# Kernel optimization log

Measured on AMD Instinct MI355X. Metric: run time of the kernel, lower is better.

## Reference

```python
import jax, jax.numpy as jnp
import numpy as np

B, D, N, H = 1024, 512, 16, 512  # batch, latent, branches, hidden


def _lrelu(v):
    return jnp.where(v >= 0, v, 0.1 * v)  # LeakyReLU(0.1)


def setup_inputs() -> dict:
    key = jax.random.key(0)
    ks = jax.random.split(key, 9)
    s = 0.02
    return {
        "x": jax.random.normal(ks[0], (B, D, N), dtype=jnp.float32),
        "Ws1": jax.random.normal(ks[1], (D, D), dtype=jnp.float32) * s,
        "bs1": jnp.zeros((D,), dtype=jnp.float32),
        "Ws2": jax.random.normal(ks[2], (D, D), dtype=jnp.float32) * s,
        "bs2": jnp.zeros((D,), dtype=jnp.float32),
        # per-branch binary classifiers: Linear(D,H)+LeakyReLU+Linear(H,1)
        "Wc1": jax.random.normal(ks[3], (N, D, H), dtype=jnp.float32) * s,
        "bc1": jnp.zeros((N, H), dtype=jnp.float32),
        "Wc2": jax.random.normal(ks[4], (N, H), dtype=jnp.float32) * s,
        "bc2": jnp.zeros((N,), dtype=jnp.float32),
    }


def reference(x, Ws1, bs1, Ws2, bs2, Wc1, bc1, Wc2, bc2):
    # x: [B, D, N] -> per-branch tokens [B, N, D]
    xb = jnp.transpose(x, (0, 2, 1))
    # shared MLP applied to every branch slice (same weights)
    h = _lrelu(xb @ Ws1 + bs1)
    shared = _lrelu(h @ Ws2 + bs2)  # [B, N, D]
    # per-branch classifier on its own branch slice -> sigmoid probs
    h1 = _lrelu(jnp.einsum('bnd,ndh->bnh', shared, Wc1) + bc1)
    logits = jnp.einsum('bnh,nh->bn', h1, Wc2) + bc2  # [B, N]
    out = jax.nn.sigmoid(logits)[:, None, :]  # [B, 1, N]
    # full pass: concat branch slices along batch (branch-major), every
    # classifier applied to the full stack -> raw logits
    full_in = jnp.transpose(shared, (1, 0, 2)).reshape(N * B, D)  # [M, D]
    h2 = _lrelu(jnp.einsum('md,ndh->mnh', full_in, Wc1) + bc1)  # [M, N, H]
    full_logits = jnp.einsum('mnh,nh->mn', h2, Wc2) + bc2  # [M, N]
    full_out = full_logits[:, None, :]  # [N*B, 1, N]
    return (out, full_out)
```

## Files before the change

### kernel.cpp

```cpp
#include <hip/hip_runtime.h>
#include <hip/hip_bf16.h>
#include <stdint.h>

#define Bq 1024
#define Dq 512
#define Nq 16
#define Hq 512
#define Mq (Bq*Nq)

typedef short v8s  __attribute__((ext_vector_type(8)));
typedef float v4f  __attribute__((ext_vector_type(4)));
typedef float v16f __attribute__((ext_vector_type(16)));

typedef __attribute__((address_space(3))) unsigned int as3_u32;
typedef __attribute__((address_space(1))) const unsigned int as1_u32;

#define VMCNT(n) asm volatile("s_waitcnt vmcnt(" #n ")" ::: "memory")

__device__ __forceinline__ unsigned short f2bf(float f) {
  union { float f; unsigned u; } v; v.f = f;
  return (unsigned short)((v.u + 0x7fffu + ((v.u >> 16) & 1u)) >> 16);
}

__global__ void k_transpose_x(const float* __restrict__ x, unsigned short* __restrict__ xb) {
  __shared__ float lds[Dq][Nq + 1];
  const int b = blockIdx.x;
  const float* xi = x + (size_t)b * Dq * Nq;
  const int t = threadIdx.x;
  for (int p = 0; p < (Dq*Nq)/256; ++p) {
    int i = t + p*256;
    lds[i >> 4][i & (Nq-1)] = xi[i];
  }
  __syncthreads();
  unsigned short* o = xb + (size_t)b * Nq * Dq;
  for (int p = 0; p < (Dq*Nq)/256; ++p) {
    int i = t + p*256;
    o[i] = f2bf(lds[i & (Dq-1)][i >> 9]);
  }
}

__global__ void k_transpose_w(const float* __restrict__ Ws1, const float* __restrict__ Ws2,
                              const float* __restrict__ Wc1,
                              unsigned short* __restrict__ Ws1t, unsigned short* __restrict__ Ws2t,
                              unsigned short* __restrict__ Wc1t) {
  __shared__ float tile[32][33];
  const int z = blockIdx.z;
  const float* in;
  unsigned short* out;
  if (z == 0)      { in = Ws1; out = Ws1t; }
  else if (z == 1) { in = Ws2; out = Ws2t; }
  else             { in = Wc1 + (size_t)(z-2) * 512 * 512; out = Wc1t + (size_t)(z-2) * 512 * 512; }
  const int tx = threadIdx.x, ty = threadIdx.y;
  const int c0 = blockIdx.x * 32, r0 = blockIdx.y * 32;
#pragma unroll
  for (int j = 0; j < 4; ++j)
    tile[ty + j*8][tx] = in[(size_t)(r0 + ty + j*8) * 512 + c0 + tx];
  __syncthreads();
#pragma unroll
  for (int j = 0; j < 4; ++j) {
    int c = c0 + ty + j*8;
    int r = r0 + tx;
    out[(size_t)c * 512 + r] = f2bf(tile[tx][ty + j*8]);
  }
}

template<int MODE, int BM>
__global__ __launch_bounds__(256, 2)
void k_gemm(const unsigned short* __restrict__ A,
            const unsigned short* __restrict__ Bt,
            const float* __restrict__ bias,
            void* __restrict__ out_,
            const float* __restrict__ w2,
            int permute) {
  constexpr int BN = 128, BK = 32, KD = 512;
  constexpr int NI = (BM == 256) ? 4 : 2;
  constexpr int AG = BM / 16;
  constexpr int TG = AG + BN / 16;
  __shared__ __align__(16) unsigned short As[2][BM][BK];
  __shared__ __align__(16) unsigned short Bs[2][BN][BK];

  const int t = threadIdx.x;
  const int wave = t >> 6, lane = t & 63;
  const int wr = (BM == 256) ? wave : (wave >> 1);
  const int wc = (BM == 256) ? 0    : (wave & 1);
  const int l32 = lane & 31, kh0 = lane >> 5;
  const int bm = blockIdx.x * BM, bn = blockIdx.y * BN;
  const int z = blockIdx.z;

  const unsigned short* Bz = Bt + (size_t)z * KD * 512;
  const float* biasz = bias + (size_t)z * 512;

  const int lrow = lane >> 2;
  const int lslot = lane & 3;

  auto stage = [&](int buf, int kt) {
#pragma unroll
    for (int i = wave; i < TG; i += 4) {
      const int isA = (i < AG);
      const int r0 = (isA ? i : i - AG) * 16;
      const int row = r0 + lrow;
      const int cg = lslot ^ ((row >> 1) & 3);
      const unsigned short* g = isA ? &A [(size_t)(bm + row) * KD + kt*BK + cg*8]
                                    : &Bz[(size_t)(bn + row) * KD + kt*BK + cg*8];
      as3_u32* d = isA ? (as3_u32*)&As[buf][r0][0] : (as3_u32*)&Bs[buf][r0][0];
      __builtin_amdgcn_global_load_lds((as1_u32*)g, d, 16, 0, 0);
    }
  };

  v16f acc[2][NI] = {};

  stage(0, 0);
  __syncthreads();

  for (int kt = 0; kt < KD / BK; ++kt) {
    const int cur = kt & 1;
    if (kt + 1 < KD / BK) stage(cur ^ 1, kt + 1);

    v8s af[2][2], bf[NI][2];
#pragma unroll
    for (int mi = 0; mi < 2; ++mi) {
      int ra = wr*64 + mi*32 + l32;
#pragma unroll
      for (int kh = 0; kh < 2; ++kh) {
        int c = kh*2 + kh0;
        af[mi][kh] = *(const v8s*)&As[cur][ra][(c ^ ((ra >> 1) & 3)) * 8];
      }
    }
#pragma unroll
    for (int ni = 0; ni < NI; ++ni) {
      int rb = wc*64 + ni*32 + l32;
#pragma unroll
      for (int kh = 0; kh < 2; ++kh) {
        int c = kh*2 + kh0;
        bf[ni][kh] = *(const v8s*)&Bs[cur][rb][(c ^ ((rb >> 1) & 3)) * 8];
      }
    }
#pragma unroll
    for (int kh = 0; kh < 2; ++kh)
#pragma unroll
      for (int mi = 0; mi < 2; ++mi)
#pragma unroll
        for (int ni = 0; ni < NI; ++ni)
          acc[mi][ni] = __builtin_amdgcn_mfma_f32_32x32x16_bf16(af[mi][kh], bf[ni][kh], acc[mi][ni], 0, 0, 0);
    __syncthreads();
  }

  if (MODE == 0) {
    unsigned short* O = (unsigned short*)out_;
#pragma unroll
    for (int mi = 0; mi < 2; ++mi) {
#pragma unroll
      for (int ni = 0; ni < NI; ++ni) {
        int col = bn + wc*64 + ni*32 + l32;
        float bcol = biasz[col];
#pragma unroll
        for (int reg = 0; reg < 16; ++reg) {
          int rl = (reg & 3) + 8*(reg >> 2) + 4*kh0;
          int grow = bm + wr*64 + mi*32 + rl;
          int orow = permute ? ((grow & 15) * Bq + (grow >> 4)) : grow;
          float v = acc[mi][ni][reg] + bcol;
          v = v >= 0.f ? v : 0.1f * v;
          O[(size_t)orow * 512 + col] = f2bf(v);
        }
      }
    }
  } else {
    float* FL = (float*)out_;
    const float* w2z = w2 + (size_t)z * 512;
#pragma unroll
    for (int mi = 0; mi < 2; ++mi) {
#pragma unroll
      for (int reg = 0; reg < 16; ++reg) {
        int rl = (reg & 3) + 8*(reg >> 2) + 4*kh0;
        float s = 0.f;
#pragma unroll
        for (int ni = 0; ni < NI; ++ni) {
          int col = bn + ni*32 + l32;
          float v = acc[mi][ni][reg] + biasz[col];
          v = v >= 0.f ? v : 0.1f * v;
          s += v * w2z[col];
        }
#pragma unroll
        for (int off = 1; off < 32; off <<= 1)
          s += __shfl_xor(s, off, 64);
        if (l32 == 0) {
          int grow = bm + wave*64 + mi*32 + rl;
          atomicAdd(&FL[(size_t)grow * Nq + z], s);
        }
      }
    }
  }
}

__global__ __launch_bounds__(256, 3)
void k_headgemm(const unsigned short* __restrict__ A,
                const unsigned short* __restrict__ Bt,
                const float* __restrict__ bias,
                float* __restrict__ FL,
                const float* __restrict__ w2) {
  __shared__ __align__(16) unsigned short As[3][128][32];
  __shared__ __align__(16) unsigned short Bs[3][128][32];

  const int t = threadIdx.x;
  const int wave = t >> 6, lane = t & 63;
  const int wr = wave >> 1, wc = wave & 1;
  const int fr = lane & 15, fq = lane >> 4;

  const int bid = blockIdx.x;
  const int lin = (bid & 7) * 1024 + (bid >> 3);
  const int bm = (lin & 127) * 128;
  const int bn = ((lin >> 7) & 3) * 128;
  const int z  = lin >> 9;

  const unsigned short* Bz = Bt + (size_t)z * Dq * 512;
  const float* biasz = bias + (size_t)z * 512;
  const float* w2z   = w2   + (size_t)z * 512;

  const int sr = lane >> 2;
  const int sc = (lane & 3) ^ ((sr >> 1) & 3);
  const unsigned short* aSrc = A  + (size_t)(bm + wave*32 + sr) * Dq + sc*8;
  const unsigned short* bSrc = Bz + (size_t)(bn + wave*32 + sr) * Dq + sc*8;
  char* dstA = (char*)As + (wave*32) * 64;
  char* dstB = (char*)Bs + (wave*32) * 64;

  auto stage = [&](int T, int slot) {
    if (T >= 16) return;
#pragma unroll
    for (int j = 0; j < 2; ++j) {
      __builtin_amdgcn_global_load_lds((as1_u32*)(aSrc + T*32 + (size_t)j*16*Dq),
                                       (as3_u32*)(dstA + slot*8192 + j*1024), 16, 0, 0);
      __builtin_amdgcn_global_load_lds((as1_u32*)(bSrc + T*32 + (size_t)j*16*Dq),
                                       (as3_u32*)(dstB + slot*8192 + j*1024), 16, 0, 0);
    }
  };

  const int swz = (fq ^ ((fr >> 1) & 3)) * 16;
  int offA[4], offB[4];
#pragma unroll
  for (int mi = 0; mi < 4; ++mi) offA[mi] = (wr*64 + mi*16 + fr) * 64 + swz;
#pragma unroll
  for (int ni = 0; ni < 4; ++ni) offB[ni] = (wc*64 + ni*16 + fr) * 64 + swz;

  v4f acc[4][4] = {};

  stage(0, 0);
  stage(1, 1);
  VMCNT(4);
  __builtin_amdgcn_s_barrier();
  __builtin_amdgcn_sched_barrier(0);

  int sR = 0, sS = 2;
  for (int kt = 0; kt < 16; ++kt) {
    stage(kt + 2, sS);

    const char* aB = (const char*)As + sR * 8192;
    const char* bB = (const char*)Bs + sR * 8192;
    v8s af[4], bf[4];
#pragma unroll
    for (int i = 0; i < 4; ++i) af[i] = *(const v8s*)(aB + offA[i]);
#pragma unroll
    for (int i = 0; i < 4; ++i) bf[i] = *(const v8s*)(bB + offB[i]);

    __builtin_amdgcn_s_setprio(1);
#pragma unroll
    for (int mi = 0; mi < 4; ++mi)
#pragma unroll
      for (int ni = 0; ni < 4; ++ni)
        acc[mi][ni] = __builtin_amdgcn_mfma_f32_16x16x32_bf16(af[mi], bf[ni], acc[mi][ni], 0, 0, 0);
    __builtin_amdgcn_s_setprio(0);

    if (kt < 14)       { VMCNT(4); }
    else if (kt == 14) { VMCNT(0); }
    if (kt < 15) {
      __builtin_amdgcn_s_barrier();
      __builtin_amdgcn_sched_barrier(0);
    }
    sR = (sR + 1 == 3) ? 0 : sR + 1;
    sS = (sS + 1 == 3) ? 0 : sS + 1;
  }

  float bcol[4], wcol[4];
#pragma unroll
  for (int ni = 0; ni < 4; ++ni) {
    int col = bn + wc*64 + ni*16 + fr;
    bcol[ni] = biasz[col];
    wcol[ni] = w2z[col];
  }
#pragma unroll
  for (int mi = 0; mi < 4; ++mi) {
#pragma unroll
    for (int reg = 0; reg < 4; ++reg) {
      float s = 0.f;
#pragma unroll
      for (int ni = 0; ni < 4; ++ni) {
        float v = acc[mi][ni][reg] + bcol[ni];
        v = v >= 0.f ? v : 0.1f * v;
        s += v * wcol[ni];
      }
#pragma unroll
      for (int off = 1; off < 16; off <<= 1)
        s += __shfl_xor(s, off, 64);
      if (fr == 0) {
        int grow = bm + wr*64 + mi*16 + fq*4 + reg;
        atomicAdd(&FL[(size_t)grow * Nq + z], s);
      }
    }
  }
}

__global__ void k_final(const float* __restrict__ fl, const float* __restrict__ bc2,
                        float* __restrict__ out) {
  int i = blockIdx.x * 256 + threadIdx.x;
  int m = i >> 4, n = i & 15;
  float v = fl[i] + bc2[n];
  out[Mq + i] = v;
  if (n == (m >> 10)) {
    int b = m & (Bq - 1);
    out[b * Nq + n] = 1.f / (1.f + __expf(-v));
  }
}

extern "C" void kernel_launch(void* const* d_in, const int* in_sizes, int n_in,
                              void* d_out, int out_size, void* d_ws, size_t ws_size,
                              hipStream_t stream) {
  (void)in_sizes; (void)n_in; (void)out_size; (void)ws_size;
  const float* x   = (const float*)d_in[0];
  const float* Ws1 = (const float*)d_in[1];
  const float* bs1 = (const float*)d_in[2];
  const float* Ws2 = (const float*)d_in[3];
  const float* bs2 = (const float*)d_in[4];
  const float* Wc1 = (const float*)d_in[5];
  const float* bc1 = (const float*)d_in[6];
  const float* Wc2 = (const float*)d_in[7];
  const float* bc2 = (const float*)d_in[8];

  char* ws = (char*)d_ws;
  unsigned short* Xb   = (unsigned short*)(ws);
  unsigned short* Hbuf = (unsigned short*)(ws + (size_t)16*1024*1024);
  unsigned short* Sm   = (unsigned short*)(ws + (size_t)32*1024*1024);
  unsigned short* Ws1t = (unsigned short*)(ws + (size_t)48*1024*1024);
  unsigned short* Ws2t = (unsigned short*)(ws + (size_t)48*1024*1024 + 512*1024);
  unsigned short* Wc1t = (unsigned short*)(ws + (size_t)49*1024*1024);
  float*          FL   = (float*)         (ws + (size_t)57*1024*1024);

  hipMemsetAsync(FL, 0, (size_t)Mq * Nq * sizeof(float), stream);

  k_transpose_x<<<Bq, 256, 0, stream>>>(x, Xb);
  k_transpose_w<<<dim3(16,16,18), dim3(32,8), 0, stream>>>(Ws1, Ws2, Wc1, Ws1t, Ws2t, Wc1t);

  k_gemm<0,128><<<dim3(128,4,1), 256, 0, stream>>>(Xb,   Ws1t, bs1, Hbuf, nullptr, 0);
  k_gemm<0,128><<<dim3(128,4,1), 256, 0, stream>>>(Hbuf, Ws2t, bs2, Sm,   nullptr, 1);
  k_headgemm<<<8192, 256, 0, stream>>>(Sm, Wc1t, bc1, FL, Wc2);

  k_final<<<(Mq*Nq)/256, 256, 0, stream>>>(FL, bc2, (float*)d_out);
}
```

Measured before the change: 351.2 us.

## Enlarge head GEMM tile to 256x128 and switch to 32x32x16 MFMA

The head GEMM block tile grows from 128x128 to 256x128, so each wave computes a 128x64 sub-tile using 32x32x16 bf16 MFMAs in place of 16x16x32. This gives more reuse of each loaded B fragment and fewer LDS reads per MFMA. The LDS double/triple buffers grow to match, and occupancy drops from 3 to 2 blocks per CU. The launch moves from an XCD-swizzled linear grid to a plain 3D grid, which may change L2 locality of the shared B tiles.

```diff
diff --git a/kernel.cpp b/kernel.cpp
--- a/kernel.cpp
+++ b/kernel.cpp
@@ -192,25 +192,23 @@
   }
 }
 
-__global__ __launch_bounds__(256, 3)
+__global__ __launch_bounds__(256, 2)
 void k_headgemm(const unsigned short* __restrict__ A,
                 const unsigned short* __restrict__ Bt,
                 const float* __restrict__ bias,
                 float* __restrict__ FL,
                 const float* __restrict__ w2) {
-  __shared__ __align__(16) unsigned short As[3][128][32];
+  __shared__ __align__(16) unsigned short As[3][256][32];
   __shared__ __align__(16) unsigned short Bs[3][128][32];
 
   const int t = threadIdx.x;
   const int wave = t >> 6, lane = t & 63;
   const int wr = wave >> 1, wc = wave & 1;
-  const int fr = lane & 15, fq = lane >> 4;
-
-  const int bid = blockIdx.x;
-  const int lin = (bid & 7) * 1024 + (bid >> 3);
-  const int bm = (lin & 127) * 128;
-  const int bn = ((lin >> 7) & 3) * 128;
-  const int z  = lin >> 9;
+  const int l32 = lane & 31, kh0 = lane >> 5;
+
+  const int bm = blockIdx.x * 256;
+  const int bn = blockIdx.y * 128;
+  const int z  = blockIdx.z;
 
   const unsigned short* Bz = Bt + (size_t)z * Dq * 512;
   const float* biasz = bias + (size_t)z * 512;
@@ -218,34 +216,44 @@
 
   const int sr = lane >> 2;
   const int sc = (lane & 3) ^ ((sr >> 1) & 3);
-  const unsigned short* aSrc = A  + (size_t)(bm + wave*32 + sr) * Dq + sc*8;
+  const unsigned short* aSrc = A  + (size_t)(bm + wave*64 + sr) * Dq + sc*8;
   const unsigned short* bSrc = Bz + (size_t)(bn + wave*32 + sr) * Dq + sc*8;
-  char* dstA = (char*)As + (wave*32) * 64;
+  char* dstA = (char*)As + (wave*64) * 64;
   char* dstB = (char*)Bs + (wave*32) * 64;
 
   auto stage = [&](int T, int slot) {
     if (T >= 16) return;
 #pragma unroll
-    for (int j = 0; j < 2; ++j) {
+    for (int j = 0; j < 4; ++j)
       __builtin_amdgcn_global_load_lds((as1_u32*)(aSrc + T*32 + (size_t)j*16*Dq),
-                                       (as3_u32*)(dstA + slot*8192 + j*1024), 16, 0, 0);
+                                       (as3_u32*)(dstA + slot*16384 + j*1024), 16, 0, 0);
+#pragma unroll
+    for (int j = 0; j < 2; ++j)
       __builtin_amdgcn_global_load_lds((as1_u32*)(bSrc + T*32 + (size_t)j*16*Dq),
                                        (as3_u32*)(dstB + slot*8192 + j*1024), 16, 0, 0);
-    }
   };
 
-  const int swz = (fq ^ ((fr >> 1) & 3)) * 16;
-  int offA[4], offB[4];
-#pragma unroll
-  for (int mi = 0; mi < 4; ++mi) offA[mi] = (wr*64 + mi*16 + fr) * 64 + swz;
-#pragma unroll
-  for (int ni = 0; ni < 4; ++ni) offB[ni] = (wc*64 + ni*16 + fr) * 64 + swz;
-
-  v4f acc[4][4] = {};
+  int offA[4][2], offB[2][2];
+#pragma unroll
+  for (int mi = 0; mi < 4; ++mi) {
+    int ra = wr*128 + mi*32 + l32;
+#pragma unroll
+    for (int kh = 0; kh < 2; ++kh)
+      offA[mi][kh] = ra*64 + (((kh*2 + kh0) ^ ((ra >> 1) & 3)) * 16);
+  }
+#pragma unroll
+  for (int ni = 0; ni < 2; ++ni) {
+    int rb = wc*64 + ni*32 + l32;
+#pragma unroll
+    for (int kh = 0; kh < 2; ++kh)
+      offB[ni][kh] = rb*64 + (((kh*2 + kh0) ^ ((rb >> 1) & 3)) * 16);
+  }
+
+  v16f acc[4][2] = {};
 
   stage(0, 0);
   stage(1, 1);
-  VMCNT(4);
+  VMCNT(6);
   __builtin_amdgcn_s_barrier();
   __builtin_amdgcn_sched_barrier(0);
 
@@ -253,23 +261,31 @@
   for (int kt = 0; kt < 16; ++kt) {
     stage(kt + 2, sS);
 
-    const char* aB = (const char*)As + sR * 8192;
+    const char* aB = (const char*)As + sR * 16384;
     const char* bB = (const char*)Bs + sR * 8192;
-    v8s af[4], bf[4];
-#pragma unroll
-    for (int i = 0; i < 4; ++i) af[i] = *(const v8s*)(aB + offA[i]);
-#pragma unroll
-    for (int i = 0; i < 4; ++i) bf[i] = *(const v8s*)(bB + offB[i]);
+    v8s af[4][2], bf[2][2];
+#pragma unroll
+    for (int mi = 0; mi < 4; ++mi)
+#pragma unroll
+      for (int kh = 0; kh < 2; ++kh)
+        af[mi][kh] = *(const v8s*)(aB + offA[mi][kh]);
+#pragma unroll
+    for (int ni = 0; ni < 2; ++ni)
+#pragma unroll
+      for (int kh = 0; kh < 2; ++kh)
+        bf[ni][kh] = *(const v8s*)(bB + offB[ni][kh]);
 
     __builtin_amdgcn_s_setprio(1);
 #pragma unroll
-    for (int mi = 0; mi < 4; ++mi)
-#pragma unroll
-      for (int ni = 0; ni < 4; ++ni)
-        acc[mi][ni] = __builtin_amdgcn_mfma_f32_16x16x32_bf16(af[mi], bf[ni], acc[mi][ni], 0, 0, 0);
+    for (int kh = 0; kh < 2; ++kh)
+#pragma unroll
+      for (int mi = 0; mi < 4; ++mi)
+#pragma unroll
+        for (int ni = 0; ni < 2; ++ni)
+          acc[mi][ni] = __builtin_amdgcn_mfma_f32_32x32x16_bf16(af[mi][kh], bf[ni][kh], acc[mi][ni], 0, 0, 0);
     __builtin_amdgcn_s_setprio(0);
 
-    if (kt < 14)       { VMCNT(4); }
+    if (kt < 14)       { VMCNT(6); }
     else if (kt == 14) { VMCNT(0); }
     if (kt < 15) {
       __builtin_amdgcn_s_barrier();
@@ -279,29 +295,30 @@
     sS = (sS + 1 == 3) ? 0 : sS + 1;
   }
 
-  float bcol[4], wcol[4];
-#pragma unroll
-  for (int ni = 0; ni < 4; ++ni) {
-    int col = bn + wc*64 + ni*16 + fr;
+  float bcol[2], wcol[2];
+#pragma unroll
+  for (int ni = 0; ni < 2; ++ni) {
+    int col = bn + wc*64 + ni*32 + l32;
     bcol[ni] = biasz[col];
     wcol[ni] = w2z[col];
   }
 #pragma unroll
   for (int mi = 0; mi < 4; ++mi) {
 #pragma unroll
-    for (int reg = 0; reg < 4; ++reg) {
+    for (int reg = 0; reg < 16; ++reg) {
+      int rl = (reg & 3) + 8*(reg >> 2) + 4*kh0;
       float s = 0.f;
 #pragma unroll
-      for (int ni = 0; ni < 4; ++ni) {
+      for (int ni = 0; ni < 2; ++ni) {
         float v = acc[mi][ni][reg] + bcol[ni];
         v = v >= 0.f ? v : 0.1f * v;
         s += v * wcol[ni];
       }
 #pragma unroll
-      for (int off = 1; off < 16; off <<= 1)
+      for (int off = 1; off < 32; off <<= 1)
         s += __shfl_xor(s, off, 64);
-      if (fr == 0) {
-        int grow = bm + wr*64 + mi*16 + fq*4 + reg;
+      if (l32 == 0) {
+        int grow = bm + wr*128 + mi*32 + rl;
         atomicAdd(&FL[(size_t)grow * Nq + z], s);
       }
     }
@@ -350,7 +367,7 @@
 
   k_gemm<0,128><<<dim3(128,4,1), 256, 0, stream>>>(Xb,   Ws1t, bs1, Hbuf, nullptr, 0);
   k_gemm<0,128><<<dim3(128,4,1), 256, 0, stream>>>(Hbuf, Ws2t, bs2, Sm,   nullptr, 1);
-  k_headgemm<<<8192, 256, 0, stream>>>(Sm, Wc1t, bc1, FL, Wc2);
+  k_headgemm<<<dim3(64,4,16), 256, 0, stream>>>(Sm, Wc1t, bc1, FL, Wc2);
 
   k_final<<<(Mq*Nq)/256, 256, 0, stream>>>(FL, bc2, (float*)d_out);
 }
```

New measurement: 448.3 us. +27.6%, slower.

## Replace triple-buffered headgemm pipeline with single-buffer BK=64 synchronous loop

Applied to the files above, without the earlier changes.

The head GEMM drops its three-slot async global-to-LDS pipeline with explicit vmcnt waits. It now uses a single 128x64 LDS tile per operand, loaded and consumed each K step between two __syncthreads, with a new XOR swizzle over 8 chunks. The block-id remap that grouped tiles by weight slice is removed in favour of a plain 3D grid, and the occupancy hint in launch_bounds is dropped. This simplifies the code and halves the number of K iterations, but it gives up overlapping loads with MFMA work and may lose L2 locality from the old tile ordering.

```diff
diff --git a/kernel.cpp b/kernel.cpp
--- a/kernel.cpp
+++ b/kernel.cpp
@@ -14,8 +14,6 @@
 
 typedef __attribute__((address_space(3))) unsigned int as3_u32;
 typedef __attribute__((address_space(1))) const unsigned int as1_u32;
-
-#define VMCNT(n) asm volatile("s_waitcnt vmcnt(" #n ")" ::: "memory")
 
 __device__ __forceinline__ unsigned short f2bf(float f) {
   union { float f; unsigned u; } v; v.f = f;
@@ -192,91 +190,80 @@
   }
 }
 
-__global__ __launch_bounds__(256, 3)
+__global__ __launch_bounds__(256)
 void k_headgemm(const unsigned short* __restrict__ A,
                 const unsigned short* __restrict__ Bt,
                 const float* __restrict__ bias,
                 float* __restrict__ FL,
                 const float* __restrict__ w2) {
-  __shared__ __align__(16) unsigned short As[3][128][32];
-  __shared__ __align__(16) unsigned short Bs[3][128][32];
+  __shared__ __align__(16) unsigned short As[128][64];
+  __shared__ __align__(16) unsigned short Bs[128][64];
 
   const int t = threadIdx.x;
   const int wave = t >> 6, lane = t & 63;
   const int wr = wave >> 1, wc = wave & 1;
   const int fr = lane & 15, fq = lane >> 4;
 
-  const int bid = blockIdx.x;
-  const int lin = (bid & 7) * 1024 + (bid >> 3);
-  const int bm = (lin & 127) * 128;
-  const int bn = ((lin >> 7) & 3) * 128;
-  const int z  = lin >> 9;
+  const int bm = blockIdx.x * 128;
+  const int bn = blockIdx.y * 128;
+  const int z  = blockIdx.z;
 
   const unsigned short* Bz = Bt + (size_t)z * Dq * 512;
   const float* biasz = bias + (size_t)z * 512;
   const float* w2z   = w2   + (size_t)z * 512;
 
-  const int sr = lane >> 2;
-  const int sc = (lane & 3) ^ ((sr >> 1) & 3);
-  const unsigned short* aSrc = A  + (size_t)(bm + wave*32 + sr) * Dq + sc*8;
-  const unsigned short* bSrc = Bz + (size_t)(bn + wave*32 + sr) * Dq + sc*8;
-  char* dstA = (char*)As + (wave*32) * 64;
-  char* dstB = (char*)Bs + (wave*32) * 64;
-
-  auto stage = [&](int T, int slot) {
-    if (T >= 16) return;
-#pragma unroll
-    for (int j = 0; j < 2; ++j) {
-      __builtin_amdgcn_global_load_lds((as1_u32*)(aSrc + T*32 + (size_t)j*16*Dq),
-                                       (as3_u32*)(dstA + slot*8192 + j*1024), 16, 0, 0);
-      __builtin_amdgcn_global_load_lds((as1_u32*)(bSrc + T*32 + (size_t)j*16*Dq),
-                                       (as3_u32*)(dstB + slot*8192 + j*1024), 16, 0, 0);
-    }
+  const int sr8 = lane >> 3;
+  const int sc8 = (lane & 7) ^ sr8;
+  const unsigned short* aSrc = A  + (size_t)(bm + wave*32 + sr8) * Dq + sc8*8;
+  const unsigned short* bSrc = Bz + (size_t)(bn + wave*32 + sr8) * Dq + sc8*8;
+
+  auto stage = [&](int kt) {
+#pragma unroll
+    for (int g = 0; g < 4; ++g)
+      __builtin_amdgcn_global_load_lds((as1_u32*)(aSrc + kt*64 + (size_t)g*8*Dq),
+                                       (as3_u32*)&As[wave*32 + g*8][0], 16, 0, 0);
+#pragma unroll
+    for (int g = 0; g < 4; ++g)
+      __builtin_amdgcn_global_load_lds((as1_u32*)(bSrc + kt*64 + (size_t)g*8*Dq),
+                                       (as3_u32*)&Bs[wave*32 + g*8][0], 16, 0, 0);
   };
 
-  const int swz = (fq ^ ((fr >> 1) & 3)) * 16;
-  int offA[4], offB[4];
-#pragma unroll
-  for (int mi = 0; mi < 4; ++mi) offA[mi] = (wr*64 + mi*16 + fr) * 64 + swz;
-#pragma unroll
-  for (int ni = 0; ni < 4; ++ni) offB[ni] = (wc*64 + ni*16 + fr) * 64 + swz;
+  int offA[4][2], offB[4][2];
+#pragma unroll
+  for (int mi = 0; mi < 4; ++mi) {
+    int r = wr*64 + mi*16 + fr;
+#pragma unroll
+    for (int kh = 0; kh < 2; ++kh)
+      offA[mi][kh] = r*128 + (((kh*4 + fq) ^ (fr & 7)) * 16);
+  }
+#pragma unroll
+  for (int ni = 0; ni < 4; ++ni) {
+    int r = wc*64 + ni*16 + fr;
+#pragma unroll
+    for (int kh = 0; kh < 2; ++kh)
+      offB[ni][kh] = r*128 + (((kh*4 + fq) ^ (fr & 7)) * 16);
+  }
 
   v4f acc[4][4] = {};
 
-  stage(0, 0);
-  stage(1, 1);
-  VMCNT(4);
-  __builtin_amdgcn_s_barrier();
-  __builtin_amdgcn_sched_barrier(0);
-
-  int sR = 0, sS = 2;
-  for (int kt = 0; kt < 16; ++kt) {
-    stage(kt + 2, sS);
-
-    const char* aB = (const char*)As + sR * 8192;
-    const char* bB = (const char*)Bs + sR * 8192;
-    v8s af[4], bf[4];
-#pragma unroll
-    for (int i = 0; i < 4; ++i) af[i] = *(const v8s*)(aB + offA[i]);
-#pragma unroll
-    for (int i = 0; i < 4; ++i) bf[i] = *(const v8s*)(bB + offB[i]);
-
-    __builtin_amdgcn_s_setprio(1);
-#pragma unroll
-    for (int mi = 0; mi < 4; ++mi)
-#pragma unroll
-      for (int ni = 0; ni < 4; ++ni)
-        acc[mi][ni] = __builtin_amdgcn_mfma_f32_16x16x32_bf16(af[mi], bf[ni], acc[mi][ni], 0, 0, 0);
-    __builtin_amdgcn_s_setprio(0);
-
-    if (kt < 14)       { VMCNT(4); }
-    else if (kt == 14) { VMCNT(0); }
-    if (kt < 15) {
-      __builtin_amdgcn_s_barrier();
-      __builtin_amdgcn_sched_barrier(0);
-    }
-    sR = (sR + 1 == 3) ? 0 : sR + 1;
-    sS = (sS + 1 == 3) ? 0 : sS + 1;
+  for (int kt = 0; kt < 8; ++kt) {
+    stage(kt);
+    __syncthreads();
+
+#pragma unroll
+    for (int kh = 0; kh < 2; ++kh) {
+      v8s af[4], bf[4];
+#pragma unroll
+      for (int mi = 0; mi < 4; ++mi) af[mi] = *(const v8s*)((const char*)As + offA[mi][kh]);
+#pragma unroll
+      for (int ni = 0; ni < 4; ++ni) bf[ni] = *(const v8s*)((const char*)Bs + offB[ni][kh]);
+#pragma unroll
+      for (int mi = 0; mi < 4; ++mi)
+#pragma unroll
+        for (int ni = 0; ni < 4; ++ni)
+          acc[mi][ni] = __builtin_amdgcn_mfma_f32_16x16x32_bf16(af[mi], bf[ni], acc[mi][ni], 0, 0, 0);
+    }
+    __syncthreads();
   }
 
   float bcol[4], wcol[4];
@@ -350,7 +337,7 @@
 
   k_gemm<0,128><<<dim3(128,4,1), 256, 0, stream>>>(Xb,   Ws1t, bs1, Hbuf, nullptr, 0);
   k_gemm<0,128><<<dim3(128,4,1), 256, 0, stream>>>(Hbuf, Ws2t, bs2, Sm,   nullptr, 1);
-  k_headgemm<<<8192, 256, 0, stream>>>(Sm, Wc1t, bc1, FL, Wc2);
+  k_headgemm<<<dim3(128,4,16), 256, 0, stream>>>(Sm, Wc1t, bc1, FL, Wc2);
 
   k_final<<<(Mq*Nq)/256, 256, 0, stream>>>(FL, bc2, (float*)d_out);
 }
```

New measurement: 321.2 us. -8.5%, faster.

## Enlarge head GEMM tile to 256x256 with 8 waves and 4-stage pipeline

Applied to the files above, without the earlier changes.

Reworks the per-branch head GEMM from 128x128 tiles with 4 waves and a 3-slot LDS ring to 256x256 tiles with 8 waves, each wave computing 128x64, and a 4-slot prefetch ring three tiles deep. The launch becomes a plain 3D grid, dropping the swizzled block-to-tile mapping. The intent is more arithmetic per byte loaded and fewer atomic adds per output row, since each block now covers twice the columns. In exchange it doubles LDS use, allows one block per CU with more registers per thread, adds an extra barrier per K step, and loses the L2-friendly block ordering.

```diff
diff --git a/kernel.cpp b/kernel.cpp
--- a/kernel.cpp
+++ b/kernel.cpp
@@ -192,91 +192,84 @@
   }
 }
 
-__global__ __launch_bounds__(256, 3)
+__global__ __launch_bounds__(512, 1)
 void k_headgemm(const unsigned short* __restrict__ A,
                 const unsigned short* __restrict__ Bt,
                 const float* __restrict__ bias,
                 float* __restrict__ FL,
                 const float* __restrict__ w2) {
-  __shared__ __align__(16) unsigned short As[3][128][32];
-  __shared__ __align__(16) unsigned short Bs[3][128][32];
+  __shared__ __align__(16) unsigned short As[4][256][32];
+  __shared__ __align__(16) unsigned short Bs[4][256][32];
 
   const int t = threadIdx.x;
   const int wave = t >> 6, lane = t & 63;
-  const int wr = wave >> 1, wc = wave & 1;
+  const int wr = wave >> 2, wc = wave & 3;
   const int fr = lane & 15, fq = lane >> 4;
 
-  const int bid = blockIdx.x;
-  const int lin = (bid & 7) * 1024 + (bid >> 3);
-  const int bm = (lin & 127) * 128;
-  const int bn = ((lin >> 7) & 3) * 128;
-  const int z  = lin >> 9;
+  const int bm = blockIdx.x * 256;
+  const int bn = blockIdx.y * 256;
+  const int z  = blockIdx.z;
 
   const unsigned short* Bz = Bt + (size_t)z * Dq * 512;
   const float* biasz = bias + (size_t)z * 512;
   const float* w2z   = w2   + (size_t)z * 512;
 
-  const int sr = lane >> 2;
-  const int sc = (lane & 3) ^ ((sr >> 1) & 3);
-  const unsigned short* aSrc = A  + (size_t)(bm + wave*32 + sr) * Dq + sc*8;
-  const unsigned short* bSrc = Bz + (size_t)(bn + wave*32 + sr) * Dq + sc*8;
-  char* dstA = (char*)As + (wave*32) * 64;
-  char* dstB = (char*)Bs + (wave*32) * 64;
-
-  auto stage = [&](int T, int slot) {
-    if (T >= 16) return;
+  const int srow = t >> 2;
+  const int schunk = (t & 3) ^ ((t >> 3) & 3);
+  const unsigned short* aS = A  + (size_t)(bm + srow) * Dq + schunk*8;
+  const unsigned short* bS = Bz + (size_t)(bn + srow) * Dq + schunk*8;
+
+  auto stageT = [&](int T) {
+    const int s = T & 3;
 #pragma unroll
     for (int j = 0; j < 2; ++j) {
-      __builtin_amdgcn_global_load_lds((as1_u32*)(aSrc + T*32 + (size_t)j*16*Dq),
-                                       (as3_u32*)(dstA + slot*8192 + j*1024), 16, 0, 0);
-      __builtin_amdgcn_global_load_lds((as1_u32*)(bSrc + T*32 + (size_t)j*16*Dq),
-                                       (as3_u32*)(dstB + slot*8192 + j*1024), 16, 0, 0);
+      __builtin_amdgcn_global_load_lds((as1_u32*)(aS + (size_t)j*128*Dq + T*32),
+                                       (as3_u32*)&As[s][j*128 + wave*16][0], 16, 0, 0);
+      __builtin_amdgcn_global_load_lds((as1_u32*)(bS + (size_t)j*128*Dq + T*32),
+                                       (as3_u32*)&Bs[s][j*128 + wave*16][0], 16, 0, 0);
     }
   };
 
   const int swz = (fq ^ ((fr >> 1) & 3)) * 16;
-  int offA[4], offB[4];
-#pragma unroll
-  for (int mi = 0; mi < 4; ++mi) offA[mi] = (wr*64 + mi*16 + fr) * 64 + swz;
-#pragma unroll
-  for (int ni = 0; ni < 4; ++ni) offB[ni] = (wc*64 + ni*16 + fr) * 64 + swz;
-
-  v4f acc[4][4] = {};
-
-  stage(0, 0);
-  stage(1, 1);
+  int offA[8], offB[4];
+#pragma unroll
+  for (int mi = 0; mi < 8; ++mi) offA[mi] = (wr*128 + mi*16 + fr) * 64 + swz;
+#pragma unroll
+  for (int ni = 0; ni < 4; ++ni) offB[ni] = (wc*64  + ni*16 + fr) * 64 + swz;
+
+  v4f acc[8][4] = {};
+
+  stageT(0); stageT(1); stageT(2);
   VMCNT(4);
   __builtin_amdgcn_s_barrier();
   __builtin_amdgcn_sched_barrier(0);
 
-  int sR = 0, sS = 2;
-  for (int kt = 0; kt < 16; ++kt) {
-    stage(kt + 2, sS);
-
-    const char* aB = (const char*)As + sR * 8192;
-    const char* bB = (const char*)Bs + sR * 8192;
-    v8s af[4], bf[4];
-#pragma unroll
-    for (int i = 0; i < 4; ++i) af[i] = *(const v8s*)(aB + offA[i]);
-#pragma unroll
-    for (int i = 0; i < 4; ++i) bf[i] = *(const v8s*)(bB + offB[i]);
+#pragma unroll 4
+  for (int T = 0; T < 16; ++T) {
+    const char* aB = (const char*)&As[T & 3][0][0];
+    const char* bB = (const char*)&Bs[T & 3][0][0];
+    v8s af[8], bf[4];
+#pragma unroll
+    for (int mi = 0; mi < 8; ++mi) af[mi] = *(const v8s*)(aB + offA[mi]);
+#pragma unroll
+    for (int ni = 0; ni < 4; ++ni) bf[ni] = *(const v8s*)(bB + offB[ni]);
+
+    if (T + 3 < 16) stageT(T + 3);
+
+    __builtin_amdgcn_s_barrier();
 
     __builtin_amdgcn_s_setprio(1);
 #pragma unroll
-    for (int mi = 0; mi < 4; ++mi)
+    for (int mi = 0; mi < 8; ++mi)
 #pragma unroll
       for (int ni = 0; ni < 4; ++ni)
         acc[mi][ni] = __builtin_amdgcn_mfma_f32_16x16x32_bf16(af[mi], bf[ni], acc[mi][ni], 0, 0, 0);
     __builtin_amdgcn_s_setprio(0);
 
-    if (kt < 14)       { VMCNT(4); }
-    else if (kt == 14) { VMCNT(0); }
-    if (kt < 15) {
-      __builtin_amdgcn_s_barrier();
-      __builtin_amdgcn_sched_barrier(0);
-    }
-    sR = (sR + 1 == 3) ? 0 : sR + 1;
-    sS = (sS + 1 == 3) ? 0 : sS + 1;
+    if (T < 14)       { VMCNT(4); }
+    else if (T == 14) { VMCNT(0); }
+    __builtin_amdgcn_s_barrier();
+    __builtin_amdgcn_sched_barrier(0);
   }
 
   float bcol[4], wcol[4];
@@ -287,7 +280,7 @@
     wcol[ni] = w2z[col];
   }
 #pragma unroll
-  for (int mi = 0; mi < 4; ++mi) {
+  for (int mi = 0; mi < 8; ++mi) {
 #pragma unroll
     for (int reg = 0; reg < 4; ++reg) {
       float s = 0.f;
@@ -301,7 +294,7 @@
       for (int off = 1; off < 16; off <<= 1)
         s += __shfl_xor(s, off, 64);
       if (fr == 0) {
-        int grow = bm + wr*64 + mi*16 + fq*4 + reg;
+        int grow = bm + wr*128 + mi*16 + fq*4 + reg;
         atomicAdd(&FL[(size_t)grow * Nq + z], s);
       }
     }
@@ -350,7 +343,7 @@
 
   k_gemm<0,128><<<dim3(128,4,1), 256, 0, stream>>>(Xb,   Ws1t, bs1, Hbuf, nullptr, 0);
   k_gemm<0,128><<<dim3(128,4,1), 256, 0, stream>>>(Hbuf, Ws2t, bs2, Sm,   nullptr, 1);
-  k_headgemm<<<8192, 256, 0, stream>>>(Sm, Wc1t, bc1, FL, Wc2);
+  k_headgemm<<<dim3(64,2,16), 512, 0, stream>>>(Sm, Wc1t, bc1, FL, Wc2);
 
   k_final<<<(Mq*Nq)/256, 256, 0, stream>>>(FL, bc2, (float*)d_out);
 }
```

After: 354.7 us. No clear change (+1.0%).
